# Kernel tuning notes

Measured on AMD Instinct MI355X. Metric: run time of the kernel, lower is better.

The kernel has to match this reference:

```python
import jax, jax.numpy as jnp
import numpy as np

HALF = 32           # (input_channels - 1) // 2
HIDDEN = 160
OUT = 32
GRU_IN = 32         # use_intensity=False -> (input_channels - 1) // 2
B, T, C = 1024, 512, 65


def setup_inputs() -> dict:
    key = jax.random.key(0)
    ks = jax.random.split(key, 10)
    times = jnp.sort(jax.random.uniform(ks[0], (T,), dtype=jnp.float32)) * 10.0
    X = jax.random.uniform(ks[1], (B, T, C), dtype=jnp.float32)
    final_index = jax.random.randint(ks[2], (B,), 0, T)
    s_ih = 1.0 / np.sqrt(HIDDEN)
    w_ih = jax.random.uniform(ks[3], (3 * HIDDEN, GRU_IN), jnp.float32, -s_ih, s_ih)
    w_hh = jax.random.uniform(ks[4], (3 * HIDDEN, HIDDEN), jnp.float32, -s_ih, s_ih)
    b_ih = jax.random.uniform(ks[5], (3 * HIDDEN,), jnp.float32, -s_ih, s_ih)
    b_hh = jax.random.uniform(ks[6], (3 * HIDDEN,), jnp.float32, -s_ih, s_ih)
    s_l = 1.0 / np.sqrt(HIDDEN)
    lin_w = jax.random.uniform(ks[7], (OUT, HIDDEN), jnp.float32, -s_l, s_l)
    lin_b = jax.random.uniform(ks[8], (OUT,), jnp.float32, -s_l, s_l)
    return {"times": times, "X": X, "final_index": final_index,
            "w_ih": w_ih, "w_hh": w_hh, "b_ih": b_ih, "b_hh": b_hh,
            "lin_w": lin_w, "lin_b": lin_b}


def _gru_cell(x, h, w_ih, w_hh, b_ih, b_hh):
    gi = x @ w_ih.T + b_ih                     # [B, 3H]
    gh = h @ w_hh.T + b_hh                     # [B, 3H]
    ir, iz, inn = jnp.split(gi, 3, axis=-1)
    hr, hz, hn = jnp.split(gh, 3, axis=-1)
    r = jax.nn.sigmoid(ir + hr)
    z = jax.nn.sigmoid(iz + hz)
    n = jnp.tanh(inn + r * hn)
    return (1.0 - z) * n + z * h


def _step(Xi, h, dt, w_ih, w_hh, b_ih, b_hh):
    # Xi: [B, C] differenced increments; channel 0 = dt increment,
    # channels 1:1+HALF = observation flags, 1+HALF: = values.
    observation = jnp.max(Xi[:, 1:1 + HALF], axis=1) > 0.5      # [B]
    Xi_piece = Xi[:, 1 + HALF:]                                  # use_intensity=False
    Xi_piece = Xi_piece.at[:, 0].add(dt)
    new_h = _gru_cell(Xi_piece, h, w_ih, w_hh, b_ih, b_hh)
    h_upd = jnp.where(observation[:, None], new_h, h)
    dt_upd = dt + jnp.where(observation, 0.0, Xi[:, 0])
    # torch skips the whole update when no sample observed this step
    any_obs = jnp.any(observation)
    h = jnp.where(any_obs, h_upd, h)
    dt = jnp.where(any_obs, dt_upd, dt)
    return h, dt


def reference(times, X, final_index, w_ih, w_hh, b_ih, b_hh, lin_w, lin_b):
    # Differencing, as in the torch forward
    Xd = X.at[:, 1:, 1:1 + HALF].add(-X[:, :-1, 1:1 + HALF])
    Xd = Xd.at[:, 0, 0].add(-times[0])
    Xd = Xd.at[:, 1:, 0].add(-times[:-1])

    z0 = jnp.zeros((B, HIDDEN), dtype=X.dtype)
    dt0 = jnp.zeros((B,), dtype=X.dtype)
    h0, dt0 = _step(Xd[:, 0], z0, dt0, w_ih, w_hh, b_ih, b_hh)

    def body(carry, Xi):
        h, dt = carry
        # evolve(h, time_diff) is identity (GRU_dt variant)
        h, dt = _step(Xi, h, dt, w_ih, w_hh, b_ih, b_hh)
        return (h, dt), h

    xs = jnp.moveaxis(Xd[:, 1:], 1, 0)                # [T-1, B, C]
    (_, _), hs = jax.lax.scan(body, (h0, dt0), xs)    # hs: [T-1, B, H]
    out = jnp.concatenate([h0[None], hs], axis=0)     # [T, B, H]
    out = jnp.moveaxis(out, 0, 1)                     # [B, T, H]
    final = jnp.take_along_axis(out, final_index[:, None, None], axis=1)[:, 0]
    return final @ lin_w.T + lin_b
```

## Files before the change

### kernel.cpp

```cpp
#include <hip/hip_runtime.h>
#include <math.h>

#define B_SZ 1024
#define T_SZ 512
#define C_CH 65
#define HID  160
#define OUTD 32
#define M_ELEM 4
#define NBLK 256
#define NTHR 640

#define LOG2E 1.4426950408889634f

#define OBS_OFF 0
#define ANY_OFF  524288
#define XD0_OFF  526336
#define S_OFF    2623488
#define WHH_OFF  6817792
#define WIH_OFF  6971392

typedef float f32x4_t __attribute__((ext_vector_type(4)));
typedef short bf16x8_t __attribute__((ext_vector_type(8)));
typedef unsigned u32x2_t __attribute__((ext_vector_type(2)));
typedef unsigned u32x4_t __attribute__((ext_vector_type(4)));
union frag_u { u32x4_t u; bf16x8_t h; };

__device__ __forceinline__ unsigned short f2bf(float x) {
  unsigned int u = __float_as_uint(x);
  unsigned int r = ((u >> 16) & 1u) + 0x7FFFu;
  return (unsigned short)((u + r) >> 16);
}
__device__ __forceinline__ unsigned cvt_pk_bf16(float lo, float hi) {
  unsigned r;
  asm("v_cvt_pk_bf16_f32 %0, %1, %2" : "=v"(r) : "v"(lo), "v"(hi));
  return r;
}
__device__ __forceinline__ float exp2_f(float x) {
  float r; asm("v_exp_f32 %0, %1" : "=v"(r) : "v"(x)); return r;
}
__device__ __forceinline__ float rcp_f(float x) {
  float r; asm("v_rcp_f32 %0, %1" : "=v"(r) : "v"(x)); return r;
}
__device__ __forceinline__ int tabf(int r) {
  return ((r & 1) << 1) | (((r >> 1) & 1) << 4);
}

__global__ void k_zero(unsigned* __restrict__ anyv) {
  int i = blockIdx.x * blockDim.x + threadIdx.x;
  if (i < T_SZ) anyv[i] = 0u;
}

__global__ __launch_bounds__(256) void k_prep(const float* __restrict__ X,
                                              const float* __restrict__ times,
                                              unsigned char* __restrict__ obs,
                                              unsigned* __restrict__ anyv,
                                              float* __restrict__ xd0) {
  const int b = blockIdx.x;
  const float* Xb = X + (size_t)b * T_SZ * C_CH;
  for (int t = threadIdx.x; t < T_SZ; t += 256) {
    const float* cur = Xb + t * C_CH;
    const float* prv = cur - C_CH;
    float m = -1e30f;
    if (t == 0) {
      #pragma unroll
      for (int c = 1; c <= 32; ++c) m = fmaxf(m, cur[c]);
    } else {
      #pragma unroll
      for (int c = 1; c <= 32; ++c) m = fmaxf(m, cur[c] - prv[c]);
    }
    unsigned char o = (m > 0.5f) ? (unsigned char)1 : (unsigned char)0;
    obs[(size_t)b * T_SZ + t] = o;
    if (o) atomicOr(&anyv[t], 1u);
    xd0[(size_t)b * T_SZ + t] = cur[0] - times[(t == 0) ? 0 : (t - 1)];
  }
}

__global__ __launch_bounds__(64) void k_dt(const unsigned char* __restrict__ obs,
                                           const unsigned* __restrict__ anyv,
                                           const float* __restrict__ xd0,
                                           const int* __restrict__ fidx,
                                           float2* __restrict__ S) {
  const int b = blockIdx.x;
  const int lane = threadIdx.x;
  const int t0 = lane * 8;
  const unsigned long long o8 =
      *(const unsigned long long*)(obs + (size_t)b * T_SZ + t0);
  const float4* xd4 = (const float4*)(xd0 + (size_t)b * T_SZ + t0);
  const float4 xa = xd4[0], xb = xd4[1];
  const uint4* av4 = (const uint4*)(anyv + t0);
  const uint4 aa = av4[0], ab = av4[1];
  const int fi = fidx[b];
  const float xv[8] = {xa.x, xa.y, xa.z, xa.w, xb.x, xb.y, xb.z, xb.w};
  const unsigned av[8] = {aa.x, aa.y, aa.z, aa.w, ab.x, ab.y, ab.z, ab.w};
  float run = 0.f;
  float dtl[8], fl[8];
  #pragma unroll
  for (int j = 0; j < 8; ++j) {
    const int o = (int)((o8 >> (8 * j)) & 0xffULL);
    const int any = (int)av[j];
    dtl[j] = run;
    if (any && !o) run += xv[j];
    fl[j] = (any && o && (t0 + j) <= fi) ? 1.f : 0.f;
  }
  float inc = run;
  #pragma unroll
  for (int off = 1; off < 64; off <<= 1) {
    float u = __shfl_up(inc, off, 64);
    if (lane >= off) inc += u;
  }
  const float excl = inc - run;
  #pragma unroll
  for (int j = 0; j < 8; ++j)
    S[(size_t)(t0 + j) * B_SZ + b] = make_float2(excl + dtl[j], fl[j]);
}

__global__ __launch_bounds__(256) void k_pack(const float* __restrict__ w_ih,
                                              const float* __restrict__ w_hh,
                                              unsigned short* __restrict__ whh_f,
                                              unsigned short* __restrict__ wih_f) {
  int i = blockIdx.x * 256 + threadIdx.x;
  if (i < 9600) {
    int l = i & 63; int kt = (i >> 6) % 5; int g = (i / 320) % 3; int q = i / 960;
    const float scl = (g < 2) ? -LOG2E : -2.f * LOG2E;
    int row = g * 160 + q * 16 + (l & 15);
    const float* src = w_hh + (size_t)row * HID + kt * 32 + (l >> 4) * 8;
    unsigned short* dst = whh_f + (size_t)i * 8;
    #pragma unroll
    for (int j = 0; j < 8; ++j) dst[j] = f2bf(scl * src[j]);
  } else if (i < 11520) {
    int i2 = i - 9600;
    int l = i2 & 63; int g = (i2 >> 6) % 3; int q = i2 / 192;
    const float scl = (g < 2) ? -LOG2E : -2.f * LOG2E;
    int row = g * 160 + q * 16 + (l & 15);
    const float* src = w_ih + (size_t)row * 32 + (l >> 4) * 8;
    unsigned short* dst = wih_f + (size_t)i2 * 8;
    #pragma unroll
    for (int j = 0; j < 8; ++j) dst[j] = f2bf(scl * src[j]);
  }
}

#define MFMA16 __builtin_amdgcn_mfma_f32_16x16x32_bf16

__global__ __launch_bounds__(NTHR) void k_scan(
    const float* __restrict__ X, const int* __restrict__ fidx,
    const float* __restrict__ w_ih,
    const float* __restrict__ b_ih, const float* __restrict__ b_hh,
    const float* __restrict__ lin_w, const float* __restrict__ lin_b,
    const float2* __restrict__ Sf,
    const unsigned short* __restrict__ whh_f, const unsigned short* __restrict__ wih_f,
    float* __restrict__ out)
{
  const int b0 = blockIdx.x * M_ELEM;
  const int tid = threadIdx.x;
  const int wid = tid >> 6;
  const int lane = tid & 63;
  const int q = wid;

  __shared__ __align__(16) unsigned short hbuf[2][800];
  __shared__ __align__(16) float hm[M_ELEM][HID];

  { unsigned* hz = (unsigned*)hbuf;
    for (int i = tid; i < 800; i += NTHR) hz[i] = 0u; }

  int maxfi = 0;
  #pragma unroll
  for (int e = 0; e < M_ELEM; ++e) maxfi = max(maxfi, fidx[b0 + e]);

  const int r16 = lane & 15;
  const int g4 = lane >> 4;
  const int elA = ((r16 >> 2) + (r16 & 3)) & 3;
  const int me = g4;

  const int rb_u16 = (elA * 96 + tabf(elA)) * 2 + g4 * 8;
  const int col = q * 16 + r16;
  const int wA_u16 = (g4 * 96 + tabf(g4)) * 2 + col;

  bf16x8_t whh_v[3][5];
  bf16x8_t wih_v[3];
  #pragma unroll
  for (int g = 0; g < 3; ++g) {
    #pragma unroll
    for (int kt = 0; kt < 5; ++kt)
      whh_v[g][kt] = *(const bf16x8_t*)(whh_f + ((size_t)((q * 3 + g) * 5 + kt) * 64 + lane) * 8);
    wih_v[g] = *(const bf16x8_t*)(wih_f + ((size_t)(q * 3 + g) * 64 + lane) * 8);
  }
  const float b_r  = -LOG2E * (b_ih[col] + b_hh[col]);
  const float b_z  = -LOG2E * (b_ih[160 + col] + b_hh[160 + col]);
  const float b_ni = -2.f * LOG2E * b_ih[320 + col];
  const float b_nh = -2.f * LOG2E * b_hh[320 + col];
  const float w0r = -LOG2E * w_ih[(size_t)col * 32];
  const float w0z = -LOG2E * w_ih[(size_t)(160 + col) * 32];
  const float w0n = -2.f * LOG2E * w_ih[(size_t)(320 + col) * 32];

  float h = 0.f;
  const f32x4_t z4 = {0.f, 0.f, 0.f, 0.f};

  const float* xrow_base =
      X + ((size_t)(b0 + elA) * T_SZ) * C_CH + 33 + (g4 * 8);

  bf16x8_t xf0, xf1;
  {
    float x0[8];
    #pragma unroll
    for (int j = 0; j < 8; ++j) x0[j] = xrow_base[j];
    unsigned* xu = (unsigned*)&xf0;
    #pragma unroll
    for (int j = 0; j < 4; ++j) xu[j] = cvt_pk_bf16(x0[2 * j], x0[2 * j + 1]);
  }
  float xb[2][8];
  float2 sb[2];
  {
    const int t1 = (1 <= maxfi) ? 1 : 0;
    const int t2 = (2 <= maxfi) ? 2 : maxfi;
    const float* xr1 = xrow_base + (size_t)t1 * C_CH;
    const float* xr2 = xrow_base + (size_t)t2 * C_CH;
    #pragma unroll
    for (int j = 0; j < 8; ++j) { xb[0][j] = xr1[j]; xb[1][j] = xr2[j]; }
    sb[0] = Sf[(size_t)t1 * B_SZ + b0 + me];
    sb[1] = Sf[(size_t)t2 * B_SZ + b0 + me];
  }
  float cr0, cz0, cn0, fl0, cr1, cz1, cn1, fl1;
  {
    const float2 s0 = Sf[b0 + me];
    cr0 = fmaf(s0.x, w0r, b_r);
    cz0 = fmaf(s0.x, w0z, b_z);
    cn0 = fmaf(s0.x, w0n, b_ni);
    fl0 = s0.y;
  }
  __syncthreads();

  const int NSTEP = (maxfi + 2) & ~1;

#define BODY(T, PB, XFI, XFO, crI, czI, cnI, flI, crO, czO, cnO, flO)      \
  {                                                                        \
                         \
    frag_u hf0, hf1, hf2, hf3, hf4;                                        \
    {                                                                      \
      const u32x2_t* hp = (const u32x2_t*)&hbuf[PB][rb_u16];               \
      u32x2_t l0 = hp[0],  u0 = hp[1];                                     \
      u32x2_t l1 = hp[8],  u1 = hp[9];                                     \
      u32x2_t l2 = hp[16], u2 = hp[17];                                    \
      u32x2_t l3 = hp[24], u3 = hp[25];                                    \
      u32x2_t l4 = hp[32], u4 = hp[33];                                    \
      hf0.u = (u32x4_t){l0.x, l0.y, u0.x, u0.y};                           \
      hf1.u = (u32x4_t){l1.x, l1.y, u1.x, u1.y};                           \
      hf2.u = (u32x4_t){l2.x, l2.y, u2.x, u2.y};                           \
      hf3.u = (u32x4_t){l3.x, l3.y, u3.x, u3.y};                           \
      hf4.u = (u32x4_t){l4.x, l4.y, u4.x, u4.y};                           \
    }                                                                      \
    \
    f32x4_t ginr = MFMA16(XFI, wih_v[0], z4, 0, 0, 0);                     \
    f32x4_t ginz = MFMA16(XFI, wih_v[1], z4, 0, 0, 0);                     \
    f32x4_t ginn = MFMA16(XFI, wih_v[2], z4, 0, 0, 0);                     \
                    \
    __builtin_amdgcn_s_setprio(1);                                         \
    f32x4_t ra  = MFMA16(hf0.h, whh_v[0][0], ginr, 0, 0, 0);               \
    f32x4_t za  = MFMA16(hf0.h, whh_v[1][0], ginz, 0, 0, 0);               \
    f32x4_t nha = MFMA16(hf0.h, whh_v[2][0], z4,   0, 0, 0);               \
    f32x4_t rb  = MFMA16(hf2.h, whh_v[0][2], z4,   0, 0, 0);               \
    f32x4_t zb  = MFMA16(hf2.h, whh_v[1][2], z4,   0, 0, 0);               \
    f32x4_t nhb = MFMA16(hf3.h, whh_v[2][3], z4,   0, 0, 0);               \
    ra  = MFMA16(hf1.h, whh_v[0][1], ra,  0, 0, 0);                        \
    za  = MFMA16(hf1.h, whh_v[1][1], za,  0, 0, 0);                        \
    nha = MFMA16(hf1.h, whh_v[2][1], nha, 0, 0, 0);                        \
    rb  = MFMA16(hf3.h, whh_v[0][3], rb,  0, 0, 0);                        \
    zb  = MFMA16(hf3.h, whh_v[1][3], zb,  0, 0, 0);                        \
    nhb = MFMA16(hf4.h, whh_v[2][4], nhb, 0, 0, 0);                        \
    nha = MFMA16(hf2.h, whh_v[2][2], nha, 0, 0, 0);                        \
    rb  = MFMA16(hf4.h, whh_v[0][4], rb,  0, 0, 0);                        \
    zb  = MFMA16(hf4.h, whh_v[1][4], zb,  0, 0, 0);                        \
    __builtin_amdgcn_s_setprio(0);                                         \
           \
    {                                                                      \
      unsigned* xu = (unsigned*)&XFO;                                      \
      xu[0] = cvt_pk_bf16(xb[PB][0], xb[PB][1]);                           \
      xu[1] = cvt_pk_bf16(xb[PB][2], xb[PB][3]);                           \
      xu[2] = cvt_pk_bf16(xb[PB][4], xb[PB][5]);                           \
      xu[3] = cvt_pk_bf16(xb[PB][6], xb[PB][7]);                           \
    }                                                                      \
    crO = fmaf(sb[PB].x, w0r, b_r);                                        \
    czO = fmaf(sb[PB].x, w0z, b_z);                                        \
    cnO = fmaf(sb[PB].x, w0n, b_ni);                                       \
    flO = sb[PB].y;                                                        \
                    \
    {                                                                      \
      const int tl = min((T) + 3, T_SZ - 1);                               \
      const float* xr = xrow_base + (size_t)tl * C_CH;                     \
      _Pragma("unroll")                                                    \
      for (int j = 0; j < 8; ++j) xb[PB][j] = xr[j];                       \
      sb[PB] = Sf[(size_t)tl * B_SZ + b0 + me];                            \
    }                                                                      \
                         \
    {                                                                      \
      const float pre_r = (ra[0] + rb[0]) + crI;                           \
      const float rr = rcp_f(1.f + exp2_f(pre_r));                         \
      const float pre_z = (za[0] + zb[0]) + czI;                           \
      const float zz = rcp_f(1.f + exp2_f(pre_z));                         \
      float u = (ginn[0] + cnI) + rr * ((nha[0] + nhb[0]) + b_nh);         \
      u = fminf(u, 60.f);                                                  \
      const float e = exp2_f(u);                                           \
      const float nn = (1.f - e) * rcp_f(1.f + e);                         \
      const float upd = nn + zz * (h - nn);                                \
      h = h + flI * (upd - h);                                             \
    }                                                                      \
                                             \
    hbuf[PB ^ 1][wA_u16] = (unsigned short)cvt_pk_bf16(h, h);              \
    __syncthreads();                                                       \
  }

  for (int t = 0; t < NSTEP; t += 2) {
    BODY(t,     0, xf0, xf1, cr0, cz0, cn0, fl0, cr1, cz1, cn1, fl1);
    BODY(t + 1, 1, xf1, xf0, cr1, cz1, cn1, fl1, cr0, cz0, cn0, fl0);
  }
#undef BODY

  hm[me][col] = h;
  __syncthreads();
  if (tid < M_ELEM * OUTD) {
    const int e = tid >> 5, o = tid & 31;
    const float4* lw = (const float4*)(lin_w + o * HID);
    const float4* hv = (const float4*)(&hm[e][0]);
    float a0 = 0.f, a1 = 0.f, a2 = 0.f, a3 = 0.f;
    #pragma unroll
    for (int k = 0; k < HID / 4; ++k) {
      float4 w = lw[k], hh = hv[k];
      a0 = fmaf(w.x, hh.x, a0); a1 = fmaf(w.y, hh.y, a1);
      a2 = fmaf(w.z, hh.z, a2); a3 = fmaf(w.w, hh.w, a3);
    }
    out[(size_t)(b0 + e) * OUTD + o] = lin_b[o] + (a0 + a1) + (a2 + a3);
  }
}

extern "C" void kernel_launch(void* const* d_in, const int* in_sizes, int n_in,
                              void* d_out, int out_size, void* d_ws, size_t ws_size,
                              hipStream_t stream) {
  const float* times = (const float*)d_in[0];
  const float* X     = (const float*)d_in[1];
  const int*   fidx  = (const int*)d_in[2];
  const float* w_ih  = (const float*)d_in[3];
  const float* w_hh  = (const float*)d_in[4];
  const float* b_ih  = (const float*)d_in[5];
  const float* b_hh  = (const float*)d_in[6];
  const float* lin_w = (const float*)d_in[7];
  const float* lin_b = (const float*)d_in[8];
  float* outp = (float*)d_out;

  unsigned char* obsb = (unsigned char*)d_ws + OBS_OFF;
  unsigned* anyv = (unsigned*)((char*)d_ws + ANY_OFF);
  float* xd0 = (float*)((char*)d_ws + XD0_OFF);
  float2* S = (float2*)((char*)d_ws + S_OFF);
  unsigned short* whh_f = (unsigned short*)((char*)d_ws + WHH_OFF);
  unsigned short* wih_f = (unsigned short*)((char*)d_ws + WIH_OFF);

  k_zero<<<1, 512, 0, stream>>>(anyv);
  k_prep<<<B_SZ, 256, 0, stream>>>(X, times, obsb, anyv, xd0);
  k_dt<<<B_SZ, 64, 0, stream>>>(obsb, anyv, xd0, fidx, S);
  k_pack<<<45, 256, 0, stream>>>(w_ih, w_hh, whh_f, wih_f);
  k_scan<<<NBLK, NTHR, 0, stream>>>(X, fidx, w_ih, b_ih, b_hh,
                                    lin_w, lin_b, S, whh_f, wih_f, outp);
}
```

Baseline: 405.3 us.

## Pre-pack X value channels to bf16 in prep kernel for scan loads

The prep kernel now writes the 32 value channels of X as a contiguous bf16 buffer, and the scan kernel loads one 16-byte bf16x8 fragment per step. This replaces eight strided fp32 loads plus the in-loop conversion. The prefetch depth drops from three steps to two, and the gate bias terms are computed inside the body rather than one step ahead. In exchange it adds an extra global write in prep and a larger workspace, and it shortens the latency hiding for the loads in the serial recurrence.

```diff
diff --git a/kernel.cpp b/kernel.cpp
--- a/kernel.cpp
+++ b/kernel.cpp
@@ -18,6 +18,7 @@
 #define S_OFF    2623488
 #define WHH_OFF  6817792
 #define WIH_OFF  6971392
+#define XPK_OFF  7002112
 
 typedef float f32x4_t __attribute__((ext_vector_type(4)));
 typedef short bf16x8_t __attribute__((ext_vector_type(8)));
@@ -54,7 +55,8 @@
                                               const float* __restrict__ times,
                                               unsigned char* __restrict__ obs,
                                               unsigned* __restrict__ anyv,
-                                              float* __restrict__ xd0) {
+                                              float* __restrict__ xd0,
+                                              unsigned short* __restrict__ xpk) {
   const int b = blockIdx.x;
   const float* Xb = X + (size_t)b * T_SZ * C_CH;
   for (int t = threadIdx.x; t < T_SZ; t += 256) {
@@ -72,6 +74,9 @@
     obs[(size_t)b * T_SZ + t] = o;
     if (o) atomicOr(&anyv[t], 1u);
     xd0[(size_t)b * T_SZ + t] = cur[0] - times[(t == 0) ? 0 : (t - 1)];
+    unsigned short* dst = xpk + ((size_t)b * T_SZ + t) * 32;
+    #pragma unroll
+    for (int c = 0; c < 32; ++c) dst[c] = f2bf(cur[33 + c]);
   }
 }
 
@@ -142,7 +147,7 @@
 #define MFMA16 __builtin_amdgcn_mfma_f32_16x16x32_bf16
 
 __global__ __launch_bounds__(NTHR) void k_scan(
-    const float* __restrict__ X, const int* __restrict__ fidx,
+    const unsigned short* __restrict__ xpk, const int* __restrict__ fidx,
     const float* __restrict__ w_ih,
     const float* __restrict__ b_ih, const float* __restrict__ b_hh,
     const float* __restrict__ lin_w, const float* __restrict__ lin_b,
@@ -195,43 +200,18 @@
   float h = 0.f;
   const f32x4_t z4 = {0.f, 0.f, 0.f, 0.f};
 
-  const float* xrow_base =
-      X + ((size_t)(b0 + elA) * T_SZ) * C_CH + 33 + (g4 * 8);
-
-  bf16x8_t xf0, xf1;
-  {
-    float x0[8];
-    #pragma unroll
-    for (int j = 0; j < 8; ++j) x0[j] = xrow_base[j];
-    unsigned* xu = (unsigned*)&xf0;
-    #pragma unroll
-    for (int j = 0; j < 4; ++j) xu[j] = cvt_pk_bf16(x0[2 * j], x0[2 * j + 1]);
-  }
-  float xb[2][8];
-  float2 sb[2];
-  {
-    const int t1 = (1 <= maxfi) ? 1 : 0;
-    const int t2 = (2 <= maxfi) ? 2 : maxfi;
-    const float* xr1 = xrow_base + (size_t)t1 * C_CH;
-    const float* xr2 = xrow_base + (size_t)t2 * C_CH;
-    #pragma unroll
-    for (int j = 0; j < 8; ++j) { xb[0][j] = xr1[j]; xb[1][j] = xr2[j]; }
-    sb[0] = Sf[(size_t)t1 * B_SZ + b0 + me];
-    sb[1] = Sf[(size_t)t2 * B_SZ + b0 + me];
-  }
-  float cr0, cz0, cn0, fl0, cr1, cz1, cn1, fl1;
-  {
-    const float2 s0 = Sf[b0 + me];
-    cr0 = fmaf(s0.x, w0r, b_r);
-    cz0 = fmaf(s0.x, w0z, b_z);
-    cn0 = fmaf(s0.x, w0n, b_ni);
-    fl0 = s0.y;
-  }
+  const unsigned short* xpk_base =
+      xpk + ((size_t)(b0 + elA) * T_SZ) * 32 + g4 * 8;
+
+  bf16x8_t xe = *(const bf16x8_t*)(xpk_base);
+  bf16x8_t xo = *(const bf16x8_t*)(xpk_base + (size_t)min(1, maxfi) * 32);
+  float2 se = Sf[b0 + me];
+  float2 so = Sf[(size_t)min(1, maxfi) * B_SZ + b0 + me];
   __syncthreads();
 
   const int NSTEP = (maxfi + 2) & ~1;
 
-#define BODY(T, PB, XFI, XFO, crI, czI, cnI, flI, crO, czO, cnO, flO)      \
+#define BODY(T, PB, XI, SI)                                                \
   {                                                                        \
                          \
     frag_u hf0, hf1, hf2, hf3, hf4;                                        \
@@ -248,10 +228,15 @@
       hf3.u = (u32x4_t){l3.x, l3.y, u3.x, u3.y};                           \
       hf4.u = (u32x4_t){l4.x, l4.y, u4.x, u4.y};                           \
     }                                                                      \
-    \
-    f32x4_t ginr = MFMA16(XFI, wih_v[0], z4, 0, 0, 0);                     \
-    f32x4_t ginz = MFMA16(XFI, wih_v[1], z4, 0, 0, 0);                     \
-    f32x4_t ginn = MFMA16(XFI, wih_v[2], z4, 0, 0, 0);                     \
+          \
+    f32x4_t ginr = MFMA16(XI, wih_v[0], z4, 0, 0, 0);                      \
+    f32x4_t ginz = MFMA16(XI, wih_v[1], z4, 0, 0, 0);                      \
+    f32x4_t ginn = MFMA16(XI, wih_v[2], z4, 0, 0, 0);                      \
+               \
+    const float crI = fmaf(SI.x, w0r, b_r);                                \
+    const float czI = fmaf(SI.x, w0z, b_z);                                \
+    const float cnI = fmaf(SI.x, w0n, b_ni);                               \
+    const float flI = SI.y;                                                \
                     \
     __builtin_amdgcn_s_setprio(1);                                         \
     f32x4_t ra  = MFMA16(hf0.h, whh_v[0][0], ginr, 0, 0, 0);               \
@@ -270,25 +255,11 @@
     rb  = MFMA16(hf4.h, whh_v[0][4], rb,  0, 0, 0);                        \
     zb  = MFMA16(hf4.h, whh_v[1][4], zb,  0, 0, 0);                        \
     __builtin_amdgcn_s_setprio(0);                                         \
-           \
+              \
     {                                                                      \
-      unsigned* xu = (unsigned*)&XFO;                                      \
-      xu[0] = cvt_pk_bf16(xb[PB][0], xb[PB][1]);                           \
-      xu[1] = cvt_pk_bf16(xb[PB][2], xb[PB][3]);                           \
-      xu[2] = cvt_pk_bf16(xb[PB][4], xb[PB][5]);                           \
-      xu[3] = cvt_pk_bf16(xb[PB][6], xb[PB][7]);                           \
-    }                                                                      \
-    crO = fmaf(sb[PB].x, w0r, b_r);                                        \
-    czO = fmaf(sb[PB].x, w0z, b_z);                                        \
-    cnO = fmaf(sb[PB].x, w0n, b_ni);                                       \
-    flO = sb[PB].y;                                                        \
-                    \
-    {                                                                      \
-      const int tl = min((T) + 3, T_SZ - 1);                               \
-      const float* xr = xrow_base + (size_t)tl * C_CH;                     \
-      _Pragma("unroll")                                                    \
-      for (int j = 0; j < 8; ++j) xb[PB][j] = xr[j];                       \
-      sb[PB] = Sf[(size_t)tl * B_SZ + b0 + me];                            \
+      const int tl = min((T) + 2, T_SZ - 1);                               \
+      XI = *(const bf16x8_t*)(xpk_base + (size_t)tl * 32);                 \
+      SI = Sf[(size_t)tl * B_SZ + b0 + me];                                \
     }                                                                      \
                          \
     {                                                                      \
@@ -309,8 +280,8 @@
   }
 
   for (int t = 0; t < NSTEP; t += 2) {
-    BODY(t,     0, xf0, xf1, cr0, cz0, cn0, fl0, cr1, cz1, cn1, fl1);
-    BODY(t + 1, 1, xf1, xf0, cr1, cz1, cn1, fl1, cr0, cz0, cn0, fl0);
+    BODY(t,     0, xe, se);
+    BODY(t + 1, 1, xo, so);
   }
 #undef BODY
 
@@ -351,11 +322,12 @@
   float2* S = (float2*)((char*)d_ws + S_OFF);
   unsigned short* whh_f = (unsigned short*)((char*)d_ws + WHH_OFF);
   unsigned short* wih_f = (unsigned short*)((char*)d_ws + WIH_OFF);
+  unsigned short* xpk = (unsigned short*)((char*)d_ws + XPK_OFF);
 
   k_zero<<<1, 512, 0, stream>>>(anyv);
-  k_prep<<<B_SZ, 256, 0, stream>>>(X, times, obsb, anyv, xd0);
+  k_prep<<<B_SZ, 256, 0, stream>>>(X, times, obsb, anyv, xd0, xpk);
   k_dt<<<B_SZ, 64, 0, stream>>>(obsb, anyv, xd0, fidx, S);
   k_pack<<<45, 256, 0, stream>>>(w_ih, w_hh, whh_f, wih_f);
-  k_scan<<<NBLK, NTHR, 0, stream>>>(X, fidx, w_ih, b_ih, b_hh,
+  k_scan<<<NBLK, NTHR, 0, stream>>>(xpk, fidx, w_ih, b_ih, b_hh,
                                     lin_w, lin_b, S, whh_f, wih_f, outp);
 }
```

Result: faster. 367.2 us (-9.4%).
